# Performance work log

Hardware: AMD Instinct MI355X
Metric: run time of the kernel (lower is better)

## Reference

```python
import jax, jax.numpy as jnp
import numpy as np
from jax import lax

EPS = 1e-15
MAX_TANH = 1.0 - 1e-5


def _artanh(x):
    x = jnp.clip(x, -MAX_TANH, MAX_TANH)
    return jnp.arctanh(x)


def mobius_add(x, y):
    # Poincare ball, c=1 (geoopt create_ball default)
    x2 = jnp.sum(x * x, axis=-1, keepdims=True)
    y2 = jnp.sum(y * y, axis=-1, keepdims=True)
    xy = jnp.sum(x * y, axis=-1, keepdims=True)
    num = (1.0 + 2.0 * xy + y2) * x + (1.0 - x2) * y
    den = 1.0 + 2.0 * xy + x2 * y2
    return num / jnp.maximum(den, EPS)


def mobius_matvec(x, W):
    # geoopt: mobius_matvec(weight.T, x) == hyperbolic version of x @ W
    x_norm = jnp.maximum(jnp.linalg.norm(x, axis=-1, keepdims=True), EPS)
    mx = x @ W
    mx_norm = jnp.maximum(jnp.linalg.norm(mx, axis=-1, keepdims=True), EPS)
    res = jnp.tanh(mx_norm / x_norm * _artanh(x_norm)) * (mx / mx_norm)
    return jnp.where(mx_norm <= 1e-10, jnp.zeros_like(res), res)


def logmap0(y):
    yn = jnp.maximum(jnp.linalg.norm(y, axis=-1, keepdims=True), EPS)
    return _artanh(yn) * y / yn


def expmap0(u):
    un = jnp.maximum(jnp.linalg.norm(u, axis=-1, keepdims=True), EPS)
    return jnp.tanh(un) * u / un


def setup_inputs() -> dict:
    key = jax.random.key(0)
    k1, k2, k3, k4 = jax.random.split(key, 4)
    N, IN, OUT, DEG = 20000, 512, 256, 16
    feat = jax.random.normal(k1, (N, IN), dtype=jnp.float32) * 0.02    # points near origin of ball
    weight = jax.random.normal(k2, (IN, OUT), dtype=jnp.float32) * (1.0 / np.sqrt(IN))
    bias = jax.random.normal(k3, (OUT,), dtype=jnp.float32) * 0.01
    src = jax.random.randint(k4, (N, DEG), 0, N, dtype=jnp.int32)      # in-neighbors per node
    return {"feat": feat, "weight": weight, "bias": bias, "src": src}


def reference(feat, weight, bias, src):
    N, deg = src.shape
    norm = jnp.asarray(deg, feat.dtype) ** -0.5  # in_degrees == deg for all nodes
    h = feat * norm
    # in_feats > out_feats branch: transform before aggregation
    h = mobius_matvec(h, weight)                 # [N, OUT]
    msgs = h[src]                                # gather mailbox [N, deg, OUT]
    # sequential left-fold with mobius_add over neighbors (non-associative)
    carry = msgs[:, 0]
    rest = jnp.moveaxis(msgs[:, 1:], 1, 0)       # [deg-1, N, OUT]

    def step(c, m):
        return mobius_add(c, m), None

    rst, _ = lax.scan(step, carry, rest)
    rst = rst * norm
    rst = mobius_add(rst, bias)
    rst = expmap0(jax.nn.relu(logmap0(rst)))     # hyperbolic relu
    return rst
```

## Files before the change

### kernel.cpp

```cpp
#include <hip/hip_runtime.h>
#include <hip/hip_fp16.h>
#include <math.h>

#define EPSF 1e-15f
#define MAX_TANH_F (1.0f - 1e-5f)
#define KDIM 512
#define NOUT 256
#define BM 32
#define BK 64

typedef __attribute__((ext_vector_type(8))) __bf16 bf16x8;
typedef __attribute__((ext_vector_type(4))) float f32x4;

__device__ __forceinline__ float artanh_clip(float x) {
    x = fminf(fmaxf(x, -MAX_TANH_F), MAX_TANH_F);
    return atanhf(x);
}

__device__ __forceinline__ void unpack2h(unsigned int u, float& a, float& b) {
    __half2 h = __builtin_bit_cast(__half2, u);
    a = __low2float(h);
    b = __high2float(h);
}

__device__ __forceinline__ bf16x8 cvt8(const float4& a, const float4& b) {
    bf16x8 r;
    r[0] = (__bf16)a.x; r[1] = (__bf16)a.y; r[2] = (__bf16)a.z; r[3] = (__bf16)a.w;
    r[4] = (__bf16)b.x; r[5] = (__bf16)b.y; r[6] = (__bf16)b.z; r[7] = (__bf16)b.w;
    return r;
}
__device__ __forceinline__ float sq8(const float4& a, const float4& b) {
    return a.x*a.x + a.y*a.y + a.z*a.z + a.w*a.w
         + b.x*b.x + b.y*b.y + b.z*b.z + b.w*b.w;
}

__global__ __launch_bounds__(64) void prep_w_kernel(
    const float* __restrict__ W, unsigned int* __restrict__ Wp)
{
    const int b = blockIdx.x;
    const int l = threadIdx.x;
    const int k0 = (b >> 4) * 32 + (l >> 4) * 8;
    const int col = (b & 15) * 16 + (l & 15);
    bf16x8 v;
    #pragma unroll
    for (int j = 0; j < 8; ++j) v[j] = (__bf16)W[(size_t)(k0 + j) * NOUT + col];
    *(uint4*)(Wp + ((size_t)b * 64 + l) * 4) = __builtin_bit_cast(uint4, v);
}

__global__ __launch_bounds__(256) void gemm_mobius_kernel(
    const float* __restrict__ feat, const uint4* __restrict__ Wp,
    __half* __restrict__ h, float* __restrict__ hnorm2,
    float scale, int N)
{
    __shared__ float lds_a[2][BM * BK];
    __shared__ float sred[4][BM];
    __shared__ float sfac[BM];
    __shared__ float sxn2[BM];

    const int tid  = threadIdx.x;
    const int wave = tid >> 6;
    const int lane = tid & 63;
    const int rr   = lane & 15;
    const int g    = lane >> 4;
    const int base = blockIdx.x * BM;

    const int srow = tid >> 3;
    const int sk   = (tid & 7) * 8;
    const int grow = base + srow;
    const float* gsrc = feat + (size_t)(grow < N ? grow : N - 1) * KDIM + sk;
    const int wslot0 = (((tid & 7) * 2)     ^ (srow & 15)) * 4;
    const int wslot1 = (((tid & 7) * 2 + 1) ^ (srow & 15)) * 4;

    f32x4 acc[2][4];
    #pragma unroll
    for (int hh = 0; hh < 2; ++hh)
        #pragma unroll
        for (int t = 0; t < 4; ++t) acc[hh][t] = (f32x4){0.f, 0.f, 0.f, 0.f};

    const uint4* wp = Wp + (size_t)wave * 4 * 64 + lane;

    uint4 B[2][4];
    #pragma unroll
    for (int p = 0; p < 2; ++p)
        #pragma unroll
        for (int t = 0; t < 4; ++t)
            B[p][t] = wp[((size_t)p * 16 + t) * 64];

    {
        float4 a = *(const float4*)(gsrc);
        float4 b = *(const float4*)(gsrc + 4);
        float* d = &lds_a[0][srow * BK];
        *(float4*)(d + wslot0) = a;
        *(float4*)(d + wslot1) = b;
    }
    __syncthreads();

    float xs0 = 0.f, xs1 = 0.f;
    float4 n0, n1;

    #pragma unroll
    for (int kk = 0; kk < 8; ++kk) {
        if (kk < 7) {
            n0 = *(const float4*)(gsrc + (kk + 1) * BK);
            n1 = *(const float4*)(gsrc + (kk + 1) * BK + 4);
        }
        const float* buf = lds_a[kk & 1];
        #pragma unroll
        for (int ss = 0; ss < 2; ++ss) {
            const int s = kk * 2 + ss;
            const int ls0 = ((ss * 8 + g * 2)     ^ rr) * 4;
            const int ls1 = ((ss * 8 + g * 2 + 1) ^ rr) * 4;
            float4 a00 = *(const float4*)(buf + rr * BK + ls0);
            float4 a01 = *(const float4*)(buf + rr * BK + ls1);
            float4 a10 = *(const float4*)(buf + (16 + rr) * BK + ls0);
            float4 a11 = *(const float4*)(buf + (16 + rr) * BK + ls1);
            xs0 += sq8(a00, a01);
            xs1 += sq8(a10, a11);
            bf16x8 ah0 = cvt8(a00, a01);
            bf16x8 ah1 = cvt8(a10, a11);
            uint4 b0 = B[s & 1][0], b1 = B[s & 1][1], b2 = B[s & 1][2], b3 = B[s & 1][3];
            if (s + 2 < 16) {
                #pragma unroll
                for (int t = 0; t < 4; ++t)
                    B[s & 1][t] = wp[((size_t)(s + 2) * 16 + t) * 64];
            }
            acc[0][0] = __builtin_amdgcn_mfma_f32_16x16x32_bf16(ah0, __builtin_bit_cast(bf16x8, b0), acc[0][0], 0, 0, 0);
            acc[1][0] = __builtin_amdgcn_mfma_f32_16x16x32_bf16(ah1, __builtin_bit_cast(bf16x8, b0), acc[1][0], 0, 0, 0);
            acc[0][1] = __builtin_amdgcn_mfma_f32_16x16x32_bf16(ah0, __builtin_bit_cast(bf16x8, b1), acc[0][1], 0, 0, 0);
            acc[1][1] = __builtin_amdgcn_mfma_f32_16x16x32_bf16(ah1, __builtin_bit_cast(bf16x8, b1), acc[1][1], 0, 0, 0);
            acc[0][2] = __builtin_amdgcn_mfma_f32_16x16x32_bf16(ah0, __builtin_bit_cast(bf16x8, b2), acc[0][2], 0, 0, 0);
            acc[1][2] = __builtin_amdgcn_mfma_f32_16x16x32_bf16(ah1, __builtin_bit_cast(bf16x8, b2), acc[1][2], 0, 0, 0);
            acc[0][3] = __builtin_amdgcn_mfma_f32_16x16x32_bf16(ah0, __builtin_bit_cast(bf16x8, b3), acc[0][3], 0, 0, 0);
            acc[1][3] = __builtin_amdgcn_mfma_f32_16x16x32_bf16(ah1, __builtin_bit_cast(bf16x8, b3), acc[1][3], 0, 0, 0);
        }
        if (kk < 7) {
            float* d = &lds_a[(kk + 1) & 1][srow * BK];
            *(float4*)(d + wslot0) = n0;
            *(float4*)(d + wslot1) = n1;
        }
        __syncthreads();
    }

    xs0 += __shfl_xor(xs0, 16); xs0 += __shfl_xor(xs0, 32);
    xs1 += __shfl_xor(xs1, 16); xs1 += __shfl_xor(xs1, 32);
    if (wave == 0 && lane < 16) { sxn2[lane] = xs0; sxn2[16 + lane] = xs1; }

    #pragma unroll
    for (int hh = 0; hh < 2; ++hh) {
        #pragma unroll
        for (int r = 0; r < 4; ++r) {
            float p = 0.f;
            #pragma unroll
            for (int t = 0; t < 4; ++t) p += acc[hh][t][r] * acc[hh][t][r];
            p += __shfl_xor(p, 1);
            p += __shfl_xor(p, 2);
            p += __shfl_xor(p, 4);
            p += __shfl_xor(p, 8);
            if (rr == 0) sred[wave][hh * 16 + g * 4 + r] = p;
        }
    }
    __syncthreads();

    if (tid < BM) {
        const int r = tid;
        const float mx2 = sred[0][r] + sred[1][r] + sred[2][r] + sred[3][r];
        const float mxn = fmaxf(scale * sqrtf(mx2), EPSF);
        const float xn  = fmaxf(scale * sqrtf(sxn2[r]), EPSF);
        float ttv = tanhf(mxn / xn * artanh_clip(xn));
        float fc  = ttv * scale / mxn;
        if (mxn <= 1e-10f) { fc = 0.f; ttv = 0.f; }
        sfac[r] = fc;
        if (base + r < N) hnorm2[base + r] = ttv * ttv;
    }
    __syncthreads();

    #pragma unroll
    for (int hh = 0; hh < 2; ++hh) {
        #pragma unroll
        for (int r = 0; r < 4; ++r) {
            const int row_r = base + hh * 16 + g * 4 + r;
            if (row_r < N) {
                const float fc = sfac[hh * 16 + g * 4 + r];
                __half* hr = h + (size_t)row_r * NOUT + wave * 64 + rr;
                #pragma unroll
                for (int t = 0; t < 4; ++t) hr[t * 16] = __float2half(acc[hh][t][r] * fc);
            }
        }
    }
}

__global__ __launch_bounds__(256) void aggregate_kernel(
    const __half* __restrict__ h, const float* __restrict__ hnorm2,
    const int* __restrict__ src, const float* __restrict__ bias,
    float* __restrict__ out, float scale, int N)
{
    const int wave = threadIdx.x >> 6;
    const int lane = threadIdx.x & 63;
    const int n0 = (blockIdx.x * 4 + wave) * 4;
    if (n0 >= N) return;
    const int g = lane >> 4;
    const int q = lane & 15;
    const int myrow = n0 + g;
    const bool rowok = myrow < N;

    size_t smax = (size_t)N * 16 - 1;
    size_t soff = (size_t)n0 * 16 + lane;
    int sidx = src[soff <= smax ? soff : smax];
    int idx[16];
    #pragma unroll
    for (int j = 0; j < 16; ++j) idx[j] = __shfl(sidx, (lane & 48) + j);

    float y2[16];
    #pragma unroll
    for (int j = 0; j < 16; ++j) y2[j] = hnorm2[idx[j]];

    uint4 cur0, cur1, nxt0, nxt1;
    {
        const uint4* hp = (const uint4*)(h + (size_t)idx[0] * NOUT);
        cur0 = hp[q * 2]; cur1 = hp[q * 2 + 1];
        const uint4* hp1 = (const uint4*)(h + (size_t)idx[1] * NOUT);
        nxt0 = hp1[q * 2]; nxt1 = hp1[q * 2 + 1];
    }
    float c[16];
    unpack2h(cur0.x, c[0], c[1]);   unpack2h(cur0.y, c[2], c[3]);
    unpack2h(cur0.z, c[4], c[5]);   unpack2h(cur0.w, c[6], c[7]);
    unpack2h(cur1.x, c[8], c[9]);   unpack2h(cur1.y, c[10], c[11]);
    unpack2h(cur1.z, c[12], c[13]); unpack2h(cur1.w, c[14], c[15]);
    float c2 = y2[0];

    #pragma unroll
    for (int j = 1; j < 16; ++j) {
        uint4 p0 = nxt0, p1 = nxt1;
        if (j + 1 < 16) {
            const uint4* hp = (const uint4*)(h + (size_t)idx[j + 1] * NOUT);
            nxt0 = hp[q * 2]; nxt1 = hp[q * 2 + 1];
        }
        float yv[16];
        unpack2h(p0.x, yv[0], yv[1]);   unpack2h(p0.y, yv[2], yv[3]);
        unpack2h(p0.z, yv[4], yv[5]);   unpack2h(p0.w, yv[6], yv[7]);
        unpack2h(p1.x, yv[8], yv[9]);   unpack2h(p1.y, yv[10], yv[11]);
        unpack2h(p1.z, yv[12], yv[13]); unpack2h(p1.w, yv[14], yv[15]);

        float xp = 0.f;
        #pragma unroll
        for (int i = 0; i < 16; ++i) xp = fmaf(c[i], yv[i], xp);
        xp += __shfl_xor(xp, 1);
        xp += __shfl_xor(xp, 2);
        xp += __shfl_xor(xp, 4);
        xp += __shfl_xor(xp, 8);
        const float xy = xp;

        const float A = 1.f + 2.f * xy + y2[j];
        const float B = 1.f - c2;
        const float den = fmaxf(1.f + 2.f * xy + c2 * y2[j], EPSF);
        const float inv = 1.f / den;
        #pragma unroll
        for (int i = 0; i < 16; ++i) c[i] = (fmaf(A, c[i], B * yv[i])) * inv;
        c2 = fmaxf((A * A * c2 + 2.f * A * B * xy + B * B * y2[j]) * (inv * inv), 0.f);
    }

    #pragma unroll
    for (int i = 0; i < 16; ++i) c[i] *= scale;
    c2 *= scale * scale;

    float bv[16];
    {
        const float4* bp = (const float4*)(bias + q * 16);
        float4 b0 = bp[0], b1 = bp[1], b2 = bp[2], b3 = bp[3];
        bv[0]=b0.x; bv[1]=b0.y; bv[2]=b0.z; bv[3]=b0.w;
        bv[4]=b1.x; bv[5]=b1.y; bv[6]=b1.z; bv[7]=b1.w;
        bv[8]=b2.x; bv[9]=b2.y; bv[10]=b2.z; bv[11]=b2.w;
        bv[12]=b3.x; bv[13]=b3.y; bv[14]=b3.z; bv[15]=b3.w;
    }
    float bp_ = 0.f, xp_ = 0.f;
    #pragma unroll
    for (int i = 0; i < 16; ++i) { bp_ = fmaf(bv[i], bv[i], bp_); xp_ = fmaf(c[i], bv[i], xp_); }
    bp_ += __shfl_xor(bp_, 1); xp_ += __shfl_xor(xp_, 1);
    bp_ += __shfl_xor(bp_, 2); xp_ += __shfl_xor(xp_, 2);
    bp_ += __shfl_xor(bp_, 4); xp_ += __shfl_xor(xp_, 4);
    bp_ += __shfl_xor(bp_, 8); xp_ += __shfl_xor(xp_, 8);
    const float bb = bp_, xy = xp_;

    const float A = 1.f + 2.f * xy + bb;
    const float B = 1.f - c2;
    const float den = fmaxf(1.f + 2.f * xy + c2 * bb, EPSF);
    const float inv = 1.f / den;
    float r4[16];
    #pragma unroll
    for (int i = 0; i < 16; ++i) r4[i] = fmaf(A, c[i], B * bv[i]) * inv;
    const float rn2 = fmaxf((A * A * c2 + 2.f * A * B * xy + B * B * bb) * (inv * inv), 0.f);

    const float rn = fmaxf(sqrtf(rn2), EPSF);
    const float lf = artanh_clip(rn) / rn;
    float u[16];
    float up = 0.f;
    #pragma unroll
    for (int i = 0; i < 16; ++i) { u[i] = fmaxf(r4[i] * lf, 0.f); up = fmaf(u[i], u[i], up); }
    up += __shfl_xor(up, 1);
    up += __shfl_xor(up, 2);
    up += __shfl_xor(up, 4);
    up += __shfl_xor(up, 8);
    const float un = fmaxf(sqrtf(up), EPSF);
    const float ef = tanhf(un) / un;

    if (rowok) {
        float* op = out + (size_t)myrow * NOUT + q * 16;
        float4 o;
        o.x = u[0]*ef;  o.y = u[1]*ef;  o.z = u[2]*ef;  o.w = u[3]*ef;  ((float4*)op)[0] = o;
        o.x = u[4]*ef;  o.y = u[5]*ef;  o.z = u[6]*ef;  o.w = u[7]*ef;  ((float4*)op)[1] = o;
        o.x = u[8]*ef;  o.y = u[9]*ef;  o.z = u[10]*ef; o.w = u[11]*ef; ((float4*)op)[2] = o;
        o.x = u[12]*ef; o.y = u[13]*ef; o.z = u[14]*ef; o.w = u[15]*ef; ((float4*)op)[3] = o;
    }
}

extern "C" void kernel_launch(void* const* d_in, const int* in_sizes, int n_in,
                              void* d_out, int out_size, void* d_ws, size_t ws_size,
                              hipStream_t stream) {
    const float* feat   = (const float*)d_in[0];
    const float* weight = (const float*)d_in[1];
    const float* bias   = (const float*)d_in[2];
    const int*   src    = (const int*)d_in[3];

    const int OUT = in_sizes[2];
    const int IN  = in_sizes[1] / OUT;
    const int N   = in_sizes[0] / IN;
    const int DEG = in_sizes[3] / N;
    (void)IN; (void)DEG; (void)out_size; (void)ws_size; (void)n_in;

    const float scale = 1.0f / sqrtf((float)DEG);

    char* ws = (char*)d_ws;
    __half* h     = (__half*)ws;
    float* hnorm2 = (float*)(ws + (size_t)N * NOUT * 2);
    unsigned int* Wp = (unsigned int*)(ws + (size_t)N * NOUT * 2 + (size_t)N * 4);

    float* out = (float*)d_out;

    const int nbm = (N + BM - 1) / BM;

    hipLaunchKernelGGL(prep_w_kernel, dim3(256), dim3(64), 0, stream,
                       weight, Wp);
    hipLaunchKernelGGL(gemm_mobius_kernel, dim3(nbm), dim3(256), 0, stream,
                       feat, (const uint4*)Wp, h, hnorm2, scale, N);
    hipLaunchKernelGGL(aggregate_kernel, dim3((N + 15) / 16), dim3(256), 0, stream,
                       h, hnorm2, src, bias, out, scale, N);
}
```

Measured before the change: 52.84 us.

## Widen GEMM block to 8 waves, deepen aggregate gather prefetch, use fast rcp

```diff
diff --git a/kernel.cpp b/kernel.cpp
--- a/kernel.cpp
+++ b/kernel.cpp
@@ -47,13 +47,13 @@
     *(uint4*)(Wp + ((size_t)b * 64 + l) * 4) = __builtin_bit_cast(uint4, v);
 }
 
-__global__ __launch_bounds__(256) void gemm_mobius_kernel(
+__global__ __launch_bounds__(512, 4) void gemm_mobius_kernel(
     const float* __restrict__ feat, const uint4* __restrict__ Wp,
     __half* __restrict__ h, float* __restrict__ hnorm2,
     float scale, int N)
 {
     __shared__ float lds_a[2][BM * BK];
-    __shared__ float sred[4][BM];
+    __shared__ float sred[8][BM];
     __shared__ float sfac[BM];
     __shared__ float sxn2[BM];
 
@@ -64,52 +64,47 @@
     const int g    = lane >> 4;
     const int base = blockIdx.x * BM;
 
-    const int srow = tid >> 3;
-    const int sk   = (tid & 7) * 8;
+    const int srow  = tid >> 4;
+    const int sslot = tid & 15;
     const int grow = base + srow;
-    const float* gsrc = feat + (size_t)(grow < N ? grow : N - 1) * KDIM + sk;
-    const int wslot0 = (((tid & 7) * 2)     ^ (srow & 15)) * 4;
-    const int wslot1 = (((tid & 7) * 2 + 1) ^ (srow & 15)) * 4;
-
-    f32x4 acc[2][4];
+    const float* gsrc = feat + (size_t)(grow < N ? grow : N - 1) * KDIM + sslot * 4;
+    const int woff = srow * BK + ((sslot ^ (srow & 15)) << 2);
+
+    f32x4 acc[2][2];
     #pragma unroll
     for (int hh = 0; hh < 2; ++hh)
         #pragma unroll
-        for (int t = 0; t < 4; ++t) acc[hh][t] = (f32x4){0.f, 0.f, 0.f, 0.f};
-
-    const uint4* wp = Wp + (size_t)wave * 4 * 64 + lane;
-
-    uint4 B[2][4];
+        for (int t = 0; t < 2; ++t) acc[hh][t] = (f32x4){0.f, 0.f, 0.f, 0.f};
+
+    const uint4* wp = Wp + lane;
+    const int tb = 2 * wave;
+
+    uint4 Bs[2][2];
     #pragma unroll
     for (int p = 0; p < 2; ++p)
         #pragma unroll
-        for (int t = 0; t < 4; ++t)
-            B[p][t] = wp[((size_t)p * 16 + t) * 64];
-
+        for (int t = 0; t < 2; ++t)
+            Bs[p][t] = wp[(size_t)(p * 16 + tb + t) * 64];
+
+    float4 nav[2];
     {
-        float4 a = *(const float4*)(gsrc);
-        float4 b = *(const float4*)(gsrc + 4);
-        float* d = &lds_a[0][srow * BK];
-        *(float4*)(d + wslot0) = a;
-        *(float4*)(d + wslot1) = b;
+        float4 v = *(const float4*)(gsrc);
+        nav[1] = *(const float4*)(gsrc + BK);
+        *(float4*)&lds_a[0][woff] = v;
     }
     __syncthreads();
 
     float xs0 = 0.f, xs1 = 0.f;
-    float4 n0, n1;
 
     #pragma unroll
     for (int kk = 0; kk < 8; ++kk) {
-        if (kk < 7) {
-            n0 = *(const float4*)(gsrc + (kk + 1) * BK);
-            n1 = *(const float4*)(gsrc + (kk + 1) * BK + 4);
-        }
+        if (kk + 2 < 8) nav[kk & 1] = *(const float4*)(gsrc + (kk + 2) * BK);
         const float* buf = lds_a[kk & 1];
         #pragma unroll
         for (int ss = 0; ss < 2; ++ss) {
             const int s = kk * 2 + ss;
-            const int ls0 = ((ss * 8 + g * 2)     ^ rr) * 4;
-            const int ls1 = ((ss * 8 + g * 2 + 1) ^ rr) * 4;
+            const int ls0 = ((ss * 8 + g * 2)     ^ rr) << 2;
+            const int ls1 = ((ss * 8 + g * 2 + 1) ^ rr) << 2;
             float4 a00 = *(const float4*)(buf + rr * BK + ls0);
             float4 a01 = *(const float4*)(buf + rr * BK + ls1);
             float4 a10 = *(const float4*)(buf + (16 + rr) * BK + ls0);
@@ -118,26 +113,17 @@
             xs1 += sq8(a10, a11);
             bf16x8 ah0 = cvt8(a00, a01);
             bf16x8 ah1 = cvt8(a10, a11);
-            uint4 b0 = B[s & 1][0], b1 = B[s & 1][1], b2 = B[s & 1][2], b3 = B[s & 1][3];
+            uint4 b0 = Bs[s & 1][0], b1 = Bs[s & 1][1];
             if (s + 2 < 16) {
-                #pragma unroll
-                for (int t = 0; t < 4; ++t)
-                    B[s & 1][t] = wp[((size_t)(s + 2) * 16 + t) * 64];
+                Bs[s & 1][0] = wp[(size_t)((s + 2) * 16 + tb) * 64];
+                Bs[s & 1][1] = wp[(size_t)((s + 2) * 16 + tb + 1) * 64];
             }
             acc[0][0] = __builtin_amdgcn_mfma_f32_16x16x32_bf16(ah0, __builtin_bit_cast(bf16x8, b0), acc[0][0], 0, 0, 0);
             acc[1][0] = __builtin_amdgcn_mfma_f32_16x16x32_bf16(ah1, __builtin_bit_cast(bf16x8, b0), acc[1][0], 0, 0, 0);
             acc[0][1] = __builtin_amdgcn_mfma_f32_16x16x32_bf16(ah0, __builtin_bit_cast(bf16x8, b1), acc[0][1], 0, 0, 0);
             acc[1][1] = __builtin_amdgcn_mfma_f32_16x16x32_bf16(ah1, __builtin_bit_cast(bf16x8, b1), acc[1][1], 0, 0, 0);
-            acc[0][2] = __builtin_amdgcn_mfma_f32_16x16x32_bf16(ah0, __builtin_bit_cast(bf16x8, b2), acc[0][2], 0, 0, 0);
-            acc[1][2] = __builtin_amdgcn_mfma_f32_16x16x32_bf16(ah1, __builtin_bit_cast(bf16x8, b2), acc[1][2], 0, 0, 0);
-            acc[0][3] = __builtin_amdgcn_mfma_f32_16x16x32_bf16(ah0, __builtin_bit_cast(bf16x8, b3), acc[0][3], 0, 0, 0);
-            acc[1][3] = __builtin_amdgcn_mfma_f32_16x16x32_bf16(ah1, __builtin_bit_cast(bf16x8, b3), acc[1][3], 0, 0, 0);
         }
-        if (kk < 7) {
-            float* d = &lds_a[(kk + 1) & 1][srow * BK];
-            *(float4*)(d + wslot0) = n0;
-            *(float4*)(d + wslot1) = n1;
-        }
+        if (kk + 1 < 8) *(float4*)&lds_a[(kk + 1) & 1][woff] = nav[(kk + 1) & 1];
         __syncthreads();
     }
 
@@ -149,9 +135,7 @@
     for (int hh = 0; hh < 2; ++hh) {
         #pragma unroll
         for (int r = 0; r < 4; ++r) {
-            float p = 0.f;
-            #pragma unroll
-            for (int t = 0; t < 4; ++t) p += acc[hh][t][r] * acc[hh][t][r];
+            float p = acc[hh][0][r] * acc[hh][0][r] + acc[hh][1][r] * acc[hh][1][r];
             p += __shfl_xor(p, 1);
             p += __shfl_xor(p, 2);
             p += __shfl_xor(p, 4);
@@ -163,7 +147,9 @@
 
     if (tid < BM) {
         const int r = tid;
-        const float mx2 = sred[0][r] + sred[1][r] + sred[2][r] + sred[3][r];
+        float mx2 = 0.f;
+        #pragma unroll
+        for (int w = 0; w < 8; ++w) mx2 += sred[w][r];
         const float mxn = fmaxf(scale * sqrtf(mx2), EPSF);
         const float xn  = fmaxf(scale * sqrtf(sxn2[r]), EPSF);
         float ttv = tanhf(mxn / xn * artanh_clip(xn));
@@ -181,9 +167,9 @@
             const int row_r = base + hh * 16 + g * 4 + r;
             if (row_r < N) {
                 const float fc = sfac[hh * 16 + g * 4 + r];
-                __half* hr = h + (size_t)row_r * NOUT + wave * 64 + rr;
-                #pragma unroll
-                for (int t = 0; t < 4; ++t) hr[t * 16] = __float2half(acc[hh][t][r] * fc);
+                __half* hr = h + (size_t)row_r * NOUT + wave * 32 + rr;
+                hr[0]  = __float2half(acc[hh][0][r] * fc);
+                hr[16] = __float2half(acc[hh][1][r] * fc);
             }
         }
     }
@@ -206,21 +192,28 @@
     size_t smax = (size_t)N * 16 - 1;
     size_t soff = (size_t)n0 * 16 + lane;
     int sidx = src[soff <= smax ? soff : smax];
+    float y2v = hnorm2[sidx];
+
     int idx[16];
-    #pragma unroll
-    for (int j = 0; j < 16; ++j) idx[j] = __shfl(sidx, (lane & 48) + j);
-
     float y2[16];
     #pragma unroll
-    for (int j = 0; j < 16; ++j) y2[j] = hnorm2[idx[j]];
-
-    uint4 cur0, cur1, nxt0, nxt1;
+    for (int j = 0; j < 16; ++j) {
+        idx[j] = __shfl(sidx, (lane & 48) + j);
+        y2[j]  = __shfl(y2v, (lane & 48) + j);
+    }
+
+    uint4 cur0, cur1;
     {
         const uint4* hp = (const uint4*)(h + (size_t)idx[0] * NOUT);
         cur0 = hp[q * 2]; cur1 = hp[q * 2 + 1];
-        const uint4* hp1 = (const uint4*)(h + (size_t)idx[1] * NOUT);
-        nxt0 = hp1[q * 2]; nxt1 = hp1[q * 2 + 1];
-    }
+    }
+    uint4 pa[4], pb[4];
+    #pragma unroll
+    for (int p = 0; p < 4; ++p) {
+        const uint4* hp = (const uint4*)(h + (size_t)idx[p + 1] * NOUT);
+        pa[p] = hp[q * 2]; pb[p] = hp[q * 2 + 1];
+    }
+
     float c[16];
     unpack2h(cur0.x, c[0], c[1]);   unpack2h(cur0.y, c[2], c[3]);
     unpack2h(cur0.z, c[4], c[5]);   unpack2h(cur0.w, c[6], c[7]);
@@ -230,10 +223,11 @@
 
     #pragma unroll
     for (int j = 1; j < 16; ++j) {
-        uint4 p0 = nxt0, p1 = nxt1;
-        if (j + 1 < 16) {
-            const uint4* hp = (const uint4*)(h + (size_t)idx[j + 1] * NOUT);
-            nxt0 = hp[q * 2]; nxt1 = hp[q * 2 + 1];
+        const int slot = (j - 1) & 3;
+        uint4 p0 = pa[slot], p1 = pb[slot];
+        if (j + 4 < 16) {
+            const uint4* hp = (const uint4*)(h + (size_t)idx[j + 4] * NOUT);
+            pa[slot] = hp[q * 2]; pb[slot] = hp[q * 2 + 1];
         }
         float yv[16];
         unpack2h(p0.x, yv[0], yv[1]);   unpack2h(p0.y, yv[2], yv[3]);
@@ -253,7 +247,7 @@
         const float A = 1.f + 2.f * xy + y2[j];
         const float B = 1.f - c2;
         const float den = fmaxf(1.f + 2.f * xy + c2 * y2[j], EPSF);
-        const float inv = 1.f / den;
+        const float inv = __builtin_amdgcn_rcpf(den);
         #pragma unroll
         for (int i = 0; i < 16; ++i) c[i] = (fmaf(A, c[i], B * yv[i])) * inv;
         c2 = fmaxf((A * A * c2 + 2.f * A * B * xy + B * B * y2[j]) * (inv * inv), 0.f);
@@ -340,7 +334,7 @@
 
     hipLaunchKernelGGL(prep_w_kernel, dim3(256), dim3(64), 0, stream,
                        weight, Wp);
-    hipLaunchKernelGGL(gemm_mobius_kernel, dim3(nbm), dim3(256), 0, stream,
+    hipLaunchKernelGGL(gemm_mobius_kernel, dim3(nbm), dim3(512), 0, stream,
                        feat, (const uint4*)Wp, h, hnorm2, scale, N);
     hipLaunchKernelGGL(aggregate_kernel, dim3((N + 15) / 16), dim3(256), 0, stream,
                        h, hnorm2, src, bias, out, scale, N);
```

New measurement: 80.57 us. 52.5% more time.
